# Kernel tuning notes

Hardware: AMD Instinct MI355X
Metric: run time of the kernel (lower is better)

The kernel has to match this reference:

```python
import jax, jax.numpy as jnp
import numpy as np
from math import log

MODEL_DIM = 512
NUM_HEADS = 8
DIM_HEAD = 64
INNER = NUM_HEADS * DIM_HEAD
B, L = 8, 1024
EPS = 1e-5


def setup_inputs() -> dict:
    key = jax.random.key(0)
    ks = jax.random.split(key, 9)
    x = jax.random.normal(ks[0], (B, L, MODEL_DIM), dtype=jnp.float32)
    gamma = jnp.ones((MODEL_DIM,), jnp.float32)
    beta = jnp.zeros((MODEL_DIM,), jnp.float32)
    w_qkv = jax.random.normal(ks[1], (3 * INNER, MODEL_DIM), jnp.float32) * (MODEL_DIM ** -0.5)
    b_qkv = jnp.zeros((3 * INNER,), jnp.float32)
    w_pos = jax.random.normal(ks[2], (INNER, MODEL_DIM), jnp.float32) * (MODEL_DIM ** -0.5)
    w_out = jax.random.normal(ks[3], (MODEL_DIM, INNER), jnp.float32) * (INNER ** -0.5)
    b_out = jnp.zeros((MODEL_DIM,), jnp.float32)
    # xavier_uniform for (num_heads, dim_head)
    bound = (6.0 / (NUM_HEADS + DIM_HEAD)) ** 0.5
    u_bias = jax.random.uniform(ks[4], (NUM_HEADS, DIM_HEAD), jnp.float32, -bound, bound)
    v_bias = jax.random.uniform(ks[5], (NUM_HEADS, DIM_HEAD), jnp.float32, -bound, bound)
    return {"x": x, "gamma": gamma, "beta": beta, "w_qkv": w_qkv, "b_qkv": b_qkv,
            "w_pos": w_pos, "w_out": w_out, "b_out": b_out, "u_bias": u_bias, "v_bias": v_bias}


def _rel_pos_emb(seq_len, d):
    # (L, D): (i - j) scaled by sinusoid frequencies, then cos on even cols, sin on odd cols
    rel = (jnp.arange(seq_len, dtype=jnp.float32)[:, None]
           - jnp.arange(d, dtype=jnp.float32)[None, :])
    freqs = jnp.exp(-jnp.arange(0, 2 * d, 2, dtype=jnp.float32) * (log(10000.0) / MODEL_DIM))
    angle = rel * freqs[None, :]
    even = (jnp.arange(d) % 2) == 0
    return jnp.where(even[None, :], jnp.cos(angle), jnp.sin(angle))  # (L, D)


def reference(x, gamma, beta, w_qkv, b_qkv, w_pos, w_out, b_out, u_bias, v_bias):
    b, l, d = x.shape
    h, dh = NUM_HEADS, DIM_HEAD
    # LayerNorm
    mu = jnp.mean(x, axis=-1, keepdims=True)
    var = jnp.mean(jnp.square(x - mu), axis=-1, keepdims=True)
    xn = (x - mu) * jax.lax.rsqrt(var + EPS) * gamma + beta
    # relative position embedding, identical per batch element
    pe = _rel_pos_emb(l, d)                      # (L, D)
    pos = (pe @ w_pos.T).reshape(l, h, dh)       # (L, H, Dh)
    pos = jnp.transpose(pos, (1, 0, 2))          # (H, L, Dh)
    # qkv
    qkv = xn @ w_qkv.T + b_qkv                   # (B, L, 3*inner)
    q, k, v = jnp.split(qkv, 3, axis=-1)
    def to_heads(t):
        return jnp.transpose(t.reshape(b, l, h, dh), (0, 2, 1, 3))  # (B,H,L,Dh)
    q, k, v = to_heads(q), to_heads(k), to_heads(v)
    scale = dh ** -0.5
    content = jnp.einsum('bhld,bhmd->bhlm', q + u_bias[None, :, None, :], k)
    pos_score = jnp.einsum('bhld,hmd->bhlm', q + v_bias[None, :, None, :], pos)
    attn = jax.nn.softmax((content + pos_score) * scale, axis=-1)
    out = jnp.einsum('bhlm,bhmd->bhld', attn, v)
    out = jnp.transpose(out, (0, 2, 1, 3)).reshape(b, l, h * dh)
    return out @ w_out.T + b_out  # dropout p=0.0 -> identity
```

## Files before the change

kernel.cpp:

```cpp
#include <hip/hip_runtime.h>
#include <math.h>

static constexpr int Bn = 8, Ln = 1024, Dm = 512, Hn = 8, DhN = 64;

typedef short bf16x8 __attribute__((ext_vector_type(8)));
typedef float f32x4 __attribute__((ext_vector_type(4)));
typedef _Float16 f16x4 __attribute__((ext_vector_type(4)));
typedef _Float16 f16x8 __attribute__((ext_vector_type(8)));
typedef unsigned int u32x4 __attribute__((ext_vector_type(4)));

#define QSCALE 0.1803368801111137f

static __device__ __forceinline__ unsigned short f2b(float f) {
  union { float f; unsigned int u; } x;
  x.f = f;
  unsigned int u = x.u;
  unsigned int r = (u + 0x7FFFu + ((u >> 16) & 1u)) >> 16;
  return (unsigned short)r;
}
static __device__ __forceinline__ float b2f(unsigned short u) {
  union { unsigned int u; float f; } x;
  x.u = ((unsigned int)u) << 16;
  return x.f;
}

#define GLDS16(g, l)                                                        \
  __builtin_amdgcn_global_load_lds((const __attribute__((address_space(1))) void*)(g), \
                                   (__attribute__((address_space(3))) void*)(l), 16, 0, 0)

__global__ __launch_bounds__(256) void prep1(const float* __restrict__ x,
                                             const float* __restrict__ gamma,
                                             const float* __restrict__ beta,
                                             unsigned short* __restrict__ xn,
                                             unsigned short* __restrict__ pe,
                                             const float* __restrict__ wq, unsigned short* __restrict__ wqb,
                                             const float* __restrict__ wp, unsigned short* __restrict__ wpb,
                                             const float* __restrict__ wo, unsigned short* __restrict__ wob) {
  int b = blockIdx.x;
  int t = threadIdx.x;
  if (b < 8192) {
    const float2 v = *(const float2*)(x + (size_t)b * Dm + t * 2);
    float s = v.x + v.y;
    float sq = v.x * v.x + v.y * v.y;
#pragma unroll
    for (int off = 32; off > 0; off >>= 1) {
      s += __shfl_down(s, off);
      sq += __shfl_down(sq, off);
    }
    __shared__ float red[8];
    int wave = t >> 6, lane = t & 63;
    if (lane == 0) { red[wave * 2] = s; red[wave * 2 + 1] = sq; }
    __syncthreads();
    float S = red[0] + red[2] + red[4] + red[6];
    float SQ = red[1] + red[3] + red[5] + red[7];
    float mu = S * (1.0f / Dm);
    float var = SQ * (1.0f / Dm) - mu * mu;
    float rstd = rsqrtf(var + 1e-5f);
    int c = t * 2;
    ushort2 o;
    o.x = f2b((v.x - mu) * rstd * gamma[c] + beta[c]);
    o.y = f2b((v.y - mu) * rstd * gamma[c + 1] + beta[c + 1]);
    *(ushort2*)(xn + (size_t)b * Dm + c) = o;
  } else if (b < 10240) {
    int idx = (b - 8192) * 256 + t;
    int l = idx >> 9, k = idx & 511;
    float freq = __expf(-0.0359778921f * (float)k);
    float angle = (float)(l - k) * freq;
    pe[idx] = f2b((k & 1) ? __sinf(angle) : __cosf(angle));
  } else {
    int cb = b - 10240;
    const float* src;
    unsigned short* dst;
    int off;
    if (cb < 768) { src = wq; dst = wqb; off = cb; }
    else if (cb < 1024) { src = wp; dst = wpb; off = cb - 768; }
    else { src = wo; dst = wob; off = cb - 1024; }
    int i = off * 256 + t;
    float4 v = *(const float4*)(src + (size_t)i * 4);
    ushort4 o;
    o.x = f2b(v.x); o.y = f2b(v.y); o.z = f2b(v.z); o.w = f2b(v.w);
    *(ushort4*)(dst + (size_t)i * 4) = o;
  }
}

__global__ __launch_bounds__(256, 6) void gemm2(const unsigned short* __restrict__ Ain,
                                                const unsigned short* __restrict__ Bwin,
                                                const float* __restrict__ biasin,
                                                unsigned short* __restrict__ oq,
                                                unsigned short* __restrict__ ok,
                                                unsigned short* __restrict__ ov,
                                                const unsigned short* __restrict__ A2,
                                                const unsigned short* __restrict__ B2,
                                                float* __restrict__ outf2) {
  int by = blockIdx.y, bx = blockIdx.x;
  int mode = 0;
  const unsigned short* A = Ain;
  const unsigned short* Bw = Bwin;
  const float* bias = biasin;
  float* outf = nullptr;
  if (by < 64) {
    int lid = by * 24 + bx;
    int i = lid >> 3;
    by = (lid & 7) * 8 + i / 24;
    bx = i % 24;
  } else {
    if (bx >= 8) return;
    A = A2; Bw = B2; bias = nullptr; outf = outf2; mode = 1; by -= 64;
  }
  const int K = 512;
  __shared__ alignas(16) unsigned short As[128 * 64];
  __shared__ alignas(16) unsigned short Bs[64 * 64];
  const int t = threadIdx.x;
  const int lane = t & 63, w = t >> 6;
  const int c = lane & 15, q8 = lane >> 4;
  const int wm = (w & 1) * 64, wn = (w >> 1) * 32;
  const int m0 = by * 128, n0 = bx * 64;

  f32x4 acc[4][2];
#pragma unroll
  for (int i = 0; i < 4; ++i)
#pragma unroll
    for (int j = 0; j < 2; ++j) acc[i][j] = (f32x4){0.f, 0.f, 0.f, 0.f};

  const int srow = lane >> 3;
  const int sgr = (lane & 7) ^ srow;

  for (int k0 = 0; k0 < K; k0 += 64) {
    __syncthreads();
#pragma unroll
    for (int s = 0; s < 4; ++s) {
      int r = s * 32 + w * 8 + srow;
      GLDS16(A + (size_t)(m0 + r) * K + k0 + sgr * 8, As + (s * 256 + w * 64 + lane) * 8);
    }
#pragma unroll
    for (int s = 0; s < 2; ++s) {
      int r = s * 32 + w * 8 + srow;
      GLDS16(Bw + (size_t)(n0 + r) * K + k0 + sgr * 8, Bs + (s * 256 + w * 64 + lane) * 8);
    }
    __syncthreads();
#pragma unroll
    for (int kk = 0; kk < 2; ++kk) {
      bf16x8 a[4], b[2];
      const int q = kk * 4 + q8;
#pragma unroll
      for (int i = 0; i < 4; ++i) {
        int r = wm + i * 16 + c;
        a[i] = *(const bf16x8*)&As[(r * 8 + (q ^ (r & 7))) * 8];
      }
#pragma unroll
      for (int j = 0; j < 2; ++j) {
        int r = wn + j * 16 + c;
        b[j] = *(const bf16x8*)&Bs[(r * 8 + (q ^ (r & 7))) * 8];
      }
#pragma unroll
      for (int i = 0; i < 4; ++i)
#pragma unroll
        for (int j = 0; j < 2; ++j)
          acc[i][j] = __builtin_amdgcn_mfma_f32_16x16x32_bf16(a[i], b[j], acc[i][j], 0, 0, 0);
    }
  }
#pragma unroll
  for (int i = 0; i < 4; ++i) {
#pragma unroll
    for (int r = 0; r < 4; ++r) {
      int m = m0 + wm + i * 16 + q8 * 4 + r;
#pragma unroll
      for (int j = 0; j < 2; ++j) {
        int n = n0 + wn + j * 16 + c;
        float val = acc[i][j][r] + (bias ? bias[n] : 0.0f);
        if (mode == 0) {
          int part = n >> 9, h = (n >> 6) & 7, dh = n & 63;
          int bb = m >> 10, l = m & 1023;
          size_t idx = (size_t)((bb * 8 + h) * 1024 + l) * 64 + dh;
          if (part == 0) {
            oq[idx] = f2b(val * QSCALE);
          } else if (part == 1) {
            ok[idx] = f2b(val);
          } else {
            union { _Float16 h; unsigned short u; } cv;
            cv.h = (_Float16)val;
            ov[idx] = cv.u;
          }
        } else {
          int h = n >> 6, dh = n & 63;
          outf[(size_t)(h * 1024 + m) * 64 + dh] = val;
        }
      }
    }
  }
}

__global__ __launch_bounds__(256, 8) void gemm_mfma(const unsigned short* __restrict__ Ain,
                                                    const unsigned short* __restrict__ Bwin,
                                                    const float* __restrict__ biasin,
                                                    float* __restrict__ outfin,
                                                    int K) {
  int by = blockIdx.y, bx = blockIdx.x;
  {
    int NBX = gridDim.x;
    int lid = by * NBX + bx;
    int i = lid >> 3;
    by = (lid & 7) * 16 + i / NBX;
    bx = i % NBX;
  }
  const unsigned short* A = Ain;
  const unsigned short* Bw = Bwin;
  const float* bias = biasin;
  float* outf = outfin;
  __shared__ alignas(16) unsigned short As[64 * 64];
  __shared__ alignas(16) unsigned short Bs[64 * 64];
  const int t = threadIdx.x;
  const int lane = t & 63, w = t >> 6;
  const int c = lane & 15, q8 = lane >> 4;
  const int wm = (w & 1) * 32, wn = (w >> 1) * 32;
  const int m0 = by * 64, n0 = bx * 64;

  f32x4 acc[2][2];
#pragma unroll
  for (int i = 0; i < 2; ++i)
#pragma unroll
    for (int j = 0; j < 2; ++j) acc[i][j] = (f32x4){0.f, 0.f, 0.f, 0.f};

  const int srow = lane >> 3;
  const int sgr = (lane & 7) ^ srow;

  for (int k0 = 0; k0 < K; k0 += 64) {
    __syncthreads();
#pragma unroll
    for (int j = 0; j < 2; ++j) {
      int r = j * 32 + w * 8 + srow;
      GLDS16(A + (size_t)(m0 + r) * K + k0 + sgr * 8, As + (j * 256 + w * 64 + lane) * 8);
      GLDS16(Bw + (size_t)(n0 + r) * K + k0 + sgr * 8, Bs + (j * 256 + w * 64 + lane) * 8);
    }
    __syncthreads();
#pragma unroll
    for (int kk = 0; kk < 2; ++kk) {
      bf16x8 a[2], b[2];
      const int q = kk * 4 + q8;
#pragma unroll
      for (int i = 0; i < 2; ++i) {
        int r = wm + i * 16 + c;
        a[i] = *(const bf16x8*)&As[(r * 8 + (q ^ (r & 7))) * 8];
      }
#pragma unroll
      for (int j = 0; j < 2; ++j) {
        int r = wn + j * 16 + c;
        b[j] = *(const bf16x8*)&Bs[(r * 8 + (q ^ (r & 7))) * 8];
      }
#pragma unroll
      for (int i = 0; i < 2; ++i)
#pragma unroll
        for (int j = 0; j < 2; ++j)
          acc[i][j] = __builtin_amdgcn_mfma_f32_16x16x32_bf16(a[i], b[j], acc[i][j], 0, 0, 0);
    }
  }
#pragma unroll
  for (int i = 0; i < 2; ++i) {
#pragma unroll
    for (int r = 0; r < 4; ++r) {
      int m = m0 + wm + i * 16 + q8 * 4 + r;
#pragma unroll
      for (int j = 0; j < 2; ++j) {
        int n = n0 + wn + j * 16 + c;
        outf[(size_t)m * 512 + n] = acc[i][j][r] + bias[n];
      }
    }
  }
}

__global__ __launch_bounds__(256) void prep2(unsigned short* __restrict__ kbuf,
                                             const float* __restrict__ pos,
                                             const float* __restrict__ ub,
                                             const float* __restrict__ vbb,
                                             float* __restrict__ biasout,
                                             const unsigned short* __restrict__ v,
                                             unsigned short* __restrict__ vt) {
  int b = blockIdx.x;
  int t = threadIdx.x;
  if (b < 16384) {
    int wave = t >> 6, lane = t & 63;
    int g = b * 4 + wave;
    int h = (g >> 10) & 7;
    int m = g & 1023;
    float kv = b2f(kbuf[(size_t)g * 64 + lane]);
    float pv = pos[(size_t)(h * 1024 + m) * 64 + lane];
    float val = ub[h * 64 + lane] * kv + vbb[h * 64 + lane] * pv;
#pragma unroll
    for (int off = 32; off > 0; off >>= 1) val += __shfl_down(val, off);
    if (lane == 0) biasout[g] = val * QSCALE;
    kbuf[(size_t)g * 64 + lane] = f2b(kv + pv);
  } else {
    __shared__ unsigned short Ts[64 * 68];
    int bb = b - 16384;
    int bh = bb >> 4, lt = bb & 15;
    const unsigned short* vg = v + (size_t)bh * 65536 + lt * 4096;
#pragma unroll
    for (int s = 0; s < 4; ++s) {
      int idx = t + s * 256;
      int r = idx >> 4, c4 = (idx & 15) << 2;
      *(ushort4*)&Ts[r * 68 + c4] = *(const ushort4*)(vg + r * 64 + c4);
    }
    __syncthreads();
#pragma unroll
    for (int s = 0; s < 4; ++s) {
      int idx = t + s * 256;
      int d = idx >> 4, l4 = (idx & 15) << 2;
      ushort4 o;
      o.x = Ts[(l4 + 0) * 68 + d];
      o.y = Ts[(l4 + 1) * 68 + d];
      o.z = Ts[(l4 + 2) * 68 + d];
      o.w = Ts[(l4 + 3) * 68 + d];
      int pb = ((l4 >> 5) & 1) * 32 + ((l4 >> 2) & 3) * 8 + ((l4 >> 4) & 1) * 4;
      *(ushort4*)(vt + (size_t)bh * 65536 + d * 1024 + lt * 64 + pb) = o;
    }
  }
}

__global__ __launch_bounds__(256, 2) void flash_mfma(const unsigned short* __restrict__ qbf,
                                                     const unsigned short* __restrict__ kbf,
                                                     const unsigned short* __restrict__ vt,
                                                     const float* __restrict__ bias,
                                                     unsigned short* __restrict__ attn_out) {
  __shared__ alignas(16) unsigned short Ks[2][64 * 64];
  __shared__ alignas(16) unsigned short Vs[2][64 * 64];
  __shared__ alignas(16) float Bls[1024];
  const int t = threadIdx.x;
  const int lane = t & 63, w = t >> 6;
  const int c = lane & 15, q8 = lane >> 4;
  const int cc7 = c & 7;
  const int lid = blockIdx.x + (blockIdx.y << 3);
  const int bh = ((lid & 7) << 3) + ((lid >> 3) & 7);
  const int qt = lid >> 6;
  const unsigned short* qg = qbf + (size_t)bh * 65536;
  const unsigned short* kg = kbf + (size_t)bh * 65536;
  const unsigned short* vg = vt + (size_t)bh * 65536;
  const float* bg = bias + (size_t)bh * 1024;

  GLDS16(bg + t * 4, Bls + t * 4);

  bf16x8 bq[2][2];
#pragma unroll
  for (int g = 0; g < 2; ++g) {
    int qlg = qt * 128 + g * 64 + w * 16 + c;
    bq[g][0] = *(const bf16x8*)(qg + (size_t)qlg * 64 + q8 * 8);
    bq[g][1] = *(const bf16x8*)(qg + (size_t)qlg * 64 + 32 + q8 * 8);
  }

  float m_st[2] = {-INFINITY, -INFINITY};
  float l_st[2] = {0.0f, 0.0f};
  f32x4 o[2][4];
#pragma unroll
  for (int g = 0; g < 2; ++g)
#pragma unroll
    for (int i = 0; i < 4; ++i) o[g][i] = (f32x4){0.f, 0.f, 0.f, 0.f};

  const int srow = lane >> 3;
  const int sgr = (lane & 7) ^ srow;
  const int r0 = w * 16 + srow;

  u32x4 pk[2][2], pv[2][2];
#pragma unroll
  for (int h = 0; h < 2; ++h)
#pragma unroll
    for (int j = 0; j < 2; ++j) {
      int r = r0 + j * 8;
      pk[h][j] = *(const u32x4*)(kg + (size_t)(h * 64 + r) * 64 + sgr * 8);
      pv[h][j] = *(const u32x4*)(vg + (size_t)r * 1024 + h * 64 + sgr * 8);
    }

  for (int it = 0; it < 8; ++it) {
    __syncthreads();
#pragma unroll
    for (int h = 0; h < 2; ++h)
#pragma unroll
      for (int j = 0; j < 2; ++j) {
        int r = r0 + j * 8;
        *(u32x4*)&Ks[h][(r * 8 + (lane & 7)) * 8] = pk[h][j];
        *(u32x4*)&Vs[h][(r * 8 + (lane & 7)) * 8] = pv[h][j];
      }
    __syncthreads();
    if (it < 7) {
#pragma unroll
      for (int h = 0; h < 2; ++h)
#pragma unroll
        for (int j = 0; j < 2; ++j) {
          int r = r0 + j * 8;
          pk[h][j] = *(const u32x4*)(kg + (size_t)((it + 1) * 128 + h * 64 + r) * 64 + sgr * 8);
          pv[h][j] = *(const u32x4*)(vg + (size_t)r * 1024 + (it + 1) * 128 + h * 64 + sgr * 8);
        }
    }

    f32x4 sc[2][2][4];
#pragma unroll
    for (int h = 0; h < 2; ++h) {
#pragma unroll
      for (int nt = 0; nt < 4; ++nt) {
        f32x4 ci = *(const f32x4*)&Bls[it * 128 + h * 64 + nt * 16 + q8 * 4];
        const int row = nt * 16 + c;
        bf16x8 ak0 = *(const bf16x8*)&Ks[h][(row * 8 + (q8 ^ cc7)) * 8];
        bf16x8 ak1 = *(const bf16x8*)&Ks[h][(row * 8 + ((q8 + 4) ^ cc7)) * 8];
#pragma unroll
        for (int g = 0; g < 2; ++g) {
          f32x4 z = __builtin_amdgcn_mfma_f32_16x16x32_bf16(ak0, bq[g][0], ci, 0, 0, 0);
          sc[g][h][nt] = __builtin_amdgcn_mfma_f32_16x16x32_bf16(ak1, bq[g][1], z, 0, 0, 0);
        }
      }
    }
    float mx[2];
#pragma unroll
    for (int g = 0; g < 2; ++g) {
      float m = sc[g][0][0][0];
#pragma unroll
      for (int h = 0; h < 2; ++h)
#pragma unroll
        for (int nt = 0; nt < 4; ++nt)
#pragma unroll
          for (int r = 0; r < 4; ++r) m = fmaxf(m, sc[g][h][nt][r]);
      mx[g] = m;
    }
    {
      float s0 = __shfl_xor(mx[0], 16);
      float s1 = __shfl_xor(mx[1], 16);
      mx[0] = fmaxf(mx[0], s0);
      mx[1] = fmaxf(mx[1], s1);
      s0 = __shfl_xor(mx[0], 32);
      s1 = __shfl_xor(mx[1], 32);
      mx[0] = fmaxf(mx[0], s0);
      mx[1] = fmaxf(mx[1], s1);
    }
    f16x8 pf8[2][2][2];
#pragma unroll
    for (int g = 0; g < 2; ++g) {
      float mn = fmaxf(m_st[g], mx[g]);
      float al = __builtin_amdgcn_exp2f(m_st[g] - mn);
      float su = 0.0f;
#pragma unroll
      for (int h = 0; h < 2; ++h)
#pragma unroll
        for (int nt = 0; nt < 4; ++nt)
#pragma unroll
          for (int r = 0; r < 4; ++r) {
            float p = __builtin_amdgcn_exp2f(sc[g][h][nt][r] - mn);
            su += p;
            pf8[g][h][nt >> 1][((nt & 1) << 2) | r] = (_Float16)p;
          }
      l_st[g] = l_st[g] * al + su;
      m_st[g] = mn;
#pragma unroll
      for (int i = 0; i < 4; ++i) o[g][i] *= al;
    }
#pragma unroll
    for (int i = 0; i < 4; ++i) {
      const int row = i * 16 + c;
#pragma unroll
      for (int h = 0; h < 2; ++h) {
        f16x8 va = *(const f16x8*)&Vs[h][(row * 8 + (q8 ^ cc7)) * 8];
        f16x8 vb = *(const f16x8*)&Vs[h][(row * 8 + ((4 + q8) ^ cc7)) * 8];
#pragma unroll
        for (int g = 0; g < 2; ++g) {
          o[g][i] = __builtin_amdgcn_mfma_f32_16x16x32_f16(va, pf8[g][h][0], o[g][i], 0, 0, 0);
          o[g][i] = __builtin_amdgcn_mfma_f32_16x16x32_f16(vb, pf8[g][h][1], o[g][i], 0, 0, 0);
        }
      }
    }
  }
  float lt0 = l_st[0], lt1 = l_st[1];
  {
    float s0 = __shfl_xor(lt0, 16);
    float s1 = __shfl_xor(lt1, 16);
    lt0 += s0; lt1 += s1;
    s0 = __shfl_xor(lt0, 32);
    s1 = __shfl_xor(lt1, 32);
    lt0 += s0; lt1 += s1;
  }
  const int bidx = bh >> 3, h = bh & 7;
#pragma unroll
  for (int g = 0; g < 2; ++g) {
    int qlg = qt * 128 + g * 64 + w * 16 + c;
    float inv = 1.0f / (g == 0 ? lt0 : lt1);
    size_t base = (size_t)(bidx * 1024 + qlg) * 512 + h * 64;
#pragma unroll
    for (int i = 0; i < 4; ++i) {
      ushort4 ov4;
      ov4.x = f2b(o[g][i][0] * inv);
      ov4.y = f2b(o[g][i][1] * inv);
      ov4.z = f2b(o[g][i][2] * inv);
      ov4.w = f2b(o[g][i][3] * inv);
      *(ushort4*)(attn_out + base + i * 16 + q8 * 4) = ov4;
    }
  }
}

extern "C" void kernel_launch(void* const* d_in, const int* in_sizes, int n_in,
                              void* d_out, int out_size, void* d_ws, size_t ws_size,
                              hipStream_t stream) {
  const float* x      = (const float*)d_in[0];
  const float* gamma  = (const float*)d_in[1];
  const float* beta   = (const float*)d_in[2];
  const float* w_qkv  = (const float*)d_in[3];
  const float* b_qkv  = (const float*)d_in[4];
  const float* w_pos  = (const float*)d_in[5];
  const float* w_out  = (const float*)d_in[6];
  const float* b_out  = (const float*)d_in[7];
  const float* u_bias = (const float*)d_in[8];
  const float* v_bias = (const float*)d_in[9];
  float* out = (float*)d_out;

  unsigned short* wsu = (unsigned short*)d_ws;
  unsigned short* xnb   = wsu;
  unsigned short* peb   = wsu + 4194304;
  unsigned short* wqkvb = wsu + 4718592;
  unsigned short* wposb = wsu + 5505024;
  unsigned short* woutb = wsu + 5767168;
  unsigned short* qbf   = wsu + 6291456;
  unsigned short* kbf   = wsu + 10485760;
  unsigned short* vbf   = wsu + 14680064;
  unsigned short* vtb   = wsu + 18874368;
  unsigned short* attnb = wsu + 23068672;
  float* posb  = (float*)(wsu + 27262976);
  float* biasb = (float*)(wsu + 28311552);

  prep1<<<11520, 256, 0, stream>>>(x, gamma, beta, xnb, peb,
                                   w_qkv, wqkvb, w_pos, wposb, w_out, woutb);
  gemm2<<<dim3(24, 72), 256, 0, stream>>>(xnb, wqkvb, b_qkv, qbf, kbf, vbf,
                                          peb, wposb, posb);
  prep2<<<17408, 256, 0, stream>>>(kbf, posb, u_bias, v_bias, biasb, vbf, vtb);
  flash_mfma<<<dim3(8, 64), 256, 0, stream>>>(qbf, kbf, vtb, biasb, attnb);
  gemm_mfma<<<dim3(8, 128), 256, 0, stream>>>(attnb, woutb, b_out, out, 512);
}
```

Baseline: 169.5 us.

## Fuse K+pos merge and per-key bias computation into flash attention kernel

Moves the per-key work that prep2 did (adding the positional projection to K and computing the u/v bias dot products) into the flash attention kernel's K tile staging loop. Each block now loads fp32 pos rows alongside K and computes the merged K and the bias on the fly. prep2 shrinks to the V transpose only. This removes a global read/write pass over K and the bias buffer, at the price of redundant per-block recomputation (8 query tiles per head) and extra fp32 pos loads and register pressure inside the attention loop.

```diff
diff --git a/kernel.cpp b/kernel.cpp
--- a/kernel.cpp
+++ b/kernel.cpp
@@ -268,62 +268,44 @@
   }
 }
 
-__global__ __launch_bounds__(256) void prep2(unsigned short* __restrict__ kbuf,
-                                             const float* __restrict__ pos,
-                                             const float* __restrict__ ub,
-                                             const float* __restrict__ vbb,
-                                             float* __restrict__ biasout,
-                                             const unsigned short* __restrict__ v,
+__global__ __launch_bounds__(256) void prep2(const unsigned short* __restrict__ v,
                                              unsigned short* __restrict__ vt) {
-  int b = blockIdx.x;
+  __shared__ unsigned short Ts[64 * 68];
+  int bb = blockIdx.x;
   int t = threadIdx.x;
-  if (b < 16384) {
-    int wave = t >> 6, lane = t & 63;
-    int g = b * 4 + wave;
-    int h = (g >> 10) & 7;
-    int m = g & 1023;
-    float kv = b2f(kbuf[(size_t)g * 64 + lane]);
-    float pv = pos[(size_t)(h * 1024 + m) * 64 + lane];
-    float val = ub[h * 64 + lane] * kv + vbb[h * 64 + lane] * pv;
-#pragma unroll
-    for (int off = 32; off > 0; off >>= 1) val += __shfl_down(val, off);
-    if (lane == 0) biasout[g] = val * QSCALE;
-    kbuf[(size_t)g * 64 + lane] = f2b(kv + pv);
-  } else {
-    __shared__ unsigned short Ts[64 * 68];
-    int bb = b - 16384;
-    int bh = bb >> 4, lt = bb & 15;
-    const unsigned short* vg = v + (size_t)bh * 65536 + lt * 4096;
-#pragma unroll
-    for (int s = 0; s < 4; ++s) {
-      int idx = t + s * 256;
-      int r = idx >> 4, c4 = (idx & 15) << 2;
-      *(ushort4*)&Ts[r * 68 + c4] = *(const ushort4*)(vg + r * 64 + c4);
-    }
-    __syncthreads();
-#pragma unroll
-    for (int s = 0; s < 4; ++s) {
-      int idx = t + s * 256;
-      int d = idx >> 4, l4 = (idx & 15) << 2;
-      ushort4 o;
-      o.x = Ts[(l4 + 0) * 68 + d];
-      o.y = Ts[(l4 + 1) * 68 + d];
-      o.z = Ts[(l4 + 2) * 68 + d];
-      o.w = Ts[(l4 + 3) * 68 + d];
-      int pb = ((l4 >> 5) & 1) * 32 + ((l4 >> 2) & 3) * 8 + ((l4 >> 4) & 1) * 4;
-      *(ushort4*)(vt + (size_t)bh * 65536 + d * 1024 + lt * 64 + pb) = o;
-    }
+  int bh = bb >> 4, lt = bb & 15;
+  const unsigned short* vg = v + (size_t)bh * 65536 + lt * 4096;
+#pragma unroll
+  for (int s = 0; s < 4; ++s) {
+    int idx = t + s * 256;
+    int r = idx >> 4, c4 = (idx & 15) << 2;
+    *(ushort4*)&Ts[r * 68 + c4] = *(const ushort4*)(vg + r * 64 + c4);
+  }
+  __syncthreads();
+#pragma unroll
+  for (int s = 0; s < 4; ++s) {
+    int idx = t + s * 256;
+    int d = idx >> 4, l4 = (idx & 15) << 2;
+    ushort4 o;
+    o.x = Ts[(l4 + 0) * 68 + d];
+    o.y = Ts[(l4 + 1) * 68 + d];
+    o.z = Ts[(l4 + 2) * 68 + d];
+    o.w = Ts[(l4 + 3) * 68 + d];
+    int pb = ((l4 >> 5) & 1) * 32 + ((l4 >> 2) & 3) * 8 + ((l4 >> 4) & 1) * 4;
+    *(ushort4*)(vt + (size_t)bh * 65536 + d * 1024 + lt * 64 + pb) = o;
   }
 }
 
 __global__ __launch_bounds__(256, 2) void flash_mfma(const unsigned short* __restrict__ qbf,
                                                      const unsigned short* __restrict__ kbf,
                                                      const unsigned short* __restrict__ vt,
-                                                     const float* __restrict__ bias,
+                                                     const float* __restrict__ posb,
+                                                     const float* __restrict__ ubias,
+                                                     const float* __restrict__ vbias,
                                                      unsigned short* __restrict__ attn_out) {
   __shared__ alignas(16) unsigned short Ks[2][64 * 64];
   __shared__ alignas(16) unsigned short Vs[2][64 * 64];
-  __shared__ alignas(16) float Bls[1024];
+  __shared__ alignas(16) float Bls[128];
   const int t = threadIdx.x;
   const int lane = t & 63, w = t >> 6;
   const int c = lane & 15, q8 = lane >> 4;
@@ -331,12 +313,28 @@
   const int lid = blockIdx.x + (blockIdx.y << 3);
   const int bh = ((lid & 7) << 3) + ((lid >> 3) & 7);
   const int qt = lid >> 6;
+  const int hd = bh & 7;
   const unsigned short* qg = qbf + (size_t)bh * 65536;
   const unsigned short* kg = kbf + (size_t)bh * 65536;
   const unsigned short* vg = vt + (size_t)bh * 65536;
-  const float* bg = bias + (size_t)bh * 1024;
-
-  GLDS16(bg + t * 4, Bls + t * 4);
+  const float* pg = posb + (size_t)hd * 65536;
+
+  const int srow = lane >> 3;
+  const int sgr = (lane & 7) ^ srow;
+  const int r0 = w * 16 + srow;
+
+  float uarr[8], varr[8];
+  {
+    f32x4 u0 = *(const f32x4*)(ubias + hd * 64 + sgr * 8);
+    f32x4 u1 = *(const f32x4*)(ubias + hd * 64 + sgr * 8 + 4);
+    f32x4 v0 = *(const f32x4*)(vbias + hd * 64 + sgr * 8);
+    f32x4 v1 = *(const f32x4*)(vbias + hd * 64 + sgr * 8 + 4);
+#pragma unroll
+    for (int e = 0; e < 4; ++e) {
+      uarr[e] = u0[e]; uarr[e + 4] = u1[e];
+      varr[e] = v0[e]; varr[e + 4] = v1[e];
+    }
+  }
 
   bf16x8 bq[2][2];
 #pragma unroll
@@ -354,18 +352,18 @@
 #pragma unroll
     for (int i = 0; i < 4; ++i) o[g][i] = (f32x4){0.f, 0.f, 0.f, 0.f};
 
-  const int srow = lane >> 3;
-  const int sgr = (lane & 7) ^ srow;
-  const int r0 = w * 16 + srow;
-
   u32x4 pk[2][2], pv[2][2];
+  f32x4 pp[2][2][2];
 #pragma unroll
   for (int h = 0; h < 2; ++h)
 #pragma unroll
     for (int j = 0; j < 2; ++j) {
       int r = r0 + j * 8;
-      pk[h][j] = *(const u32x4*)(kg + (size_t)(h * 64 + r) * 64 + sgr * 8);
+      int key = h * 64 + r;
+      pk[h][j] = *(const u32x4*)(kg + (size_t)key * 64 + sgr * 8);
       pv[h][j] = *(const u32x4*)(vg + (size_t)r * 1024 + h * 64 + sgr * 8);
+      pp[h][j][0] = *(const f32x4*)(pg + (size_t)key * 64 + sgr * 8);
+      pp[h][j][1] = *(const f32x4*)(pg + (size_t)key * 64 + sgr * 8 + 4);
     }
 
   for (int it = 0; it < 8; ++it) {
@@ -375,7 +373,25 @@
 #pragma unroll
       for (int j = 0; j < 2; ++j) {
         int r = r0 + j * 8;
-        *(u32x4*)&Ks[h][(r * 8 + (lane & 7)) * 8] = pk[h][j];
+        float parr[8];
+#pragma unroll
+        for (int e = 0; e < 4; ++e) { parr[e] = pp[h][j][0][e]; parr[e + 4] = pp[h][j][1][e]; }
+        unsigned int kw[4];
+        float part = 0.0f;
+#pragma unroll
+        for (int e = 0; e < 4; ++e) {
+          float k0 = b2f((unsigned short)(pk[h][j][e] & 0xffffu));
+          float k1 = b2f((unsigned short)(pk[h][j][e] >> 16));
+          float p0 = parr[2 * e], p1 = parr[2 * e + 1];
+          part += uarr[2 * e] * k0 + varr[2 * e] * p0 + uarr[2 * e + 1] * k1 + varr[2 * e + 1] * p1;
+          kw[e] = (unsigned int)f2b(k0 + p0) | ((unsigned int)f2b(k1 + p1) << 16);
+        }
+        part += __shfl_xor(part, 1);
+        part += __shfl_xor(part, 2);
+        part += __shfl_xor(part, 4);
+        if ((lane & 7) == 0) Bls[h * 64 + r] = part * QSCALE;
+        u32x4 ko = {kw[0], kw[1], kw[2], kw[3]};
+        *(u32x4*)&Ks[h][(r * 8 + (lane & 7)) * 8] = ko;
         *(u32x4*)&Vs[h][(r * 8 + (lane & 7)) * 8] = pv[h][j];
       }
     __syncthreads();
@@ -385,8 +401,11 @@
 #pragma unroll
         for (int j = 0; j < 2; ++j) {
           int r = r0 + j * 8;
-          pk[h][j] = *(const u32x4*)(kg + (size_t)((it + 1) * 128 + h * 64 + r) * 64 + sgr * 8);
+          int key = (it + 1) * 128 + h * 64 + r;
+          pk[h][j] = *(const u32x4*)(kg + (size_t)key * 64 + sgr * 8);
           pv[h][j] = *(const u32x4*)(vg + (size_t)r * 1024 + (it + 1) * 128 + h * 64 + sgr * 8);
+          pp[h][j][0] = *(const f32x4*)(pg + (size_t)key * 64 + sgr * 8);
+          pp[h][j][1] = *(const f32x4*)(pg + (size_t)key * 64 + sgr * 8 + 4);
         }
     }
 
@@ -395,7 +414,7 @@
     for (int h = 0; h < 2; ++h) {
 #pragma unroll
       for (int nt = 0; nt < 4; ++nt) {
-        f32x4 ci = *(const f32x4*)&Bls[it * 128 + h * 64 + nt * 16 + q8 * 4];
+        f32x4 ci = *(const f32x4*)&Bls[h * 64 + nt * 16 + q8 * 4];
         const int row = nt * 16 + c;
         bf16x8 ak0 = *(const bf16x8*)&Ks[h][(row * 8 + (q8 ^ cc7)) * 8];
         bf16x8 ak1 = *(const bf16x8*)&Ks[h][(row * 8 + ((q8 + 4) ^ cc7)) * 8];
@@ -473,12 +492,12 @@
     s1 = __shfl_xor(lt1, 32);
     lt0 += s0; lt1 += s1;
   }
-  const int bidx = bh >> 3, h = bh & 7;
+  const int bidx = bh >> 3;
 #pragma unroll
   for (int g = 0; g < 2; ++g) {
     int qlg = qt * 128 + g * 64 + w * 16 + c;
     float inv = 1.0f / (g == 0 ? lt0 : lt1);
-    size_t base = (size_t)(bidx * 1024 + qlg) * 512 + h * 64;
+    size_t base = (size_t)(bidx * 1024 + qlg) * 512 + hd * 64;
 #pragma unroll
     for (int i = 0; i < 4; ++i) {
       ushort4 ov4;
@@ -518,13 +537,12 @@
   unsigned short* vtb   = wsu + 18874368;
   unsigned short* attnb = wsu + 23068672;
   float* posb  = (float*)(wsu + 27262976);
-  float* biasb = (float*)(wsu + 28311552);
 
   prep1<<<11520, 256, 0, stream>>>(x, gamma, beta, xnb, peb,
                                    w_qkv, wqkvb, w_pos, wposb, w_out, woutb);
   gemm2<<<dim3(24, 72), 256, 0, stream>>>(xnb, wqkvb, b_qkv, qbf, kbf, vbf,
                                           peb, wposb, posb);
-  prep2<<<17408, 256, 0, stream>>>(kbf, posb, u_bias, v_bias, biasb, vbf, vtb);
-  flash_mfma<<<dim3(8, 64), 256, 0, stream>>>(qbf, kbf, vtb, biasb, attnb);
+  prep2<<<1024, 256, 0, stream>>>(vbf, vtb);
+  flash_mfma<<<dim3(8, 64), 256, 0, stream>>>(qbf, kbf, vtb, posb, u_bias, v_bias, attnb);
   gemm_mfma<<<dim3(8, 128), 256, 0, stream>>>(attnb, woutb, b_out, out, 512);
 }
```

Measured after the change: 172.4 us. No clear change (+1.7%).
